# Optimization experiments

Measured on AMD Instinct MI355X. Metric: run time of the kernel, lower is better.

Reference implementation:

```python
import jax, jax.numpy as jnp
import numpy as np
from jax.scipy.special import logsumexp

VOCAB, EMB, SEQ = 100000, 300, 32768
NTAGS = 14          # 12 real tags + START + STOP
START, STOP = 12, 13
NEG = -10000.0


def setup_inputs() -> dict:
    key = jax.random.key(0)
    k0, k1, k2, k3, k4 = jax.random.split(key, 5)
    sentence = jax.random.randint(k0, (SEQ,), 0, VOCAB, dtype=jnp.int32)
    tags = jax.random.randint(k1, (SEQ,), 0, 12, dtype=jnp.int32)  # real tags only
    embeddings = jax.random.normal(k2, (VOCAB, EMB), dtype=jnp.float32)
    W = jax.random.normal(k3, (NTAGS, EMB), dtype=jnp.float32)  # linear2tag, no bias
    transitions = jax.random.normal(k4, (NTAGS, NTAGS), dtype=jnp.float32)
    # match __init__: no transition into START, none out of STOP
    transitions = transitions.at[START, :].set(NEG).at[:, STOP].set(NEG)
    return {"sentence": sentence, "tags": tags, "embeddings": embeddings,
            "W": W, "transitions": transitions}


def _forward_alg(feats, transitions):
    # feats: [L, T]; transitions[next, prev]
    init = jnp.full((NTAGS,), NEG, feats.dtype).at[START].set(0.0)

    def step(fv, feat):
        # alphas[next, prev] = fv[prev] + trans[next, prev] + feat[next]
        alphas = fv[None, :] + transitions + feat[:, None]
        return logsumexp(alphas, axis=1), None

    fv, _ = jax.lax.scan(step, init, feats)
    return logsumexp(fv + transitions[STOP])


def _score_sentence(feats, transitions, tags):
    prev = jnp.concatenate([jnp.array([START], tags.dtype), tags[:-1]])
    trans_score = jnp.sum(transitions[tags, prev])
    emit_score = jnp.sum(jnp.take_along_axis(feats, tags[:, None].astype(jnp.int32), axis=1))
    return trans_score + emit_score + transitions[STOP, tags[-1]]


def _viterbi(feats, transitions):
    init = jnp.full((NTAGS,), NEG, feats.dtype).at[START].set(0.0)

    def step(fv, feat):
        nv = fv[None, :] + transitions          # [next, prev]
        bp = jnp.argmax(nv, axis=1)             # best prev for each next
        return jnp.max(nv, axis=1) + feat, bp

    fv, bps = jax.lax.scan(step, init, feats)   # bps: [L, T]
    terminal = fv + transitions[STOP]
    best_last = jnp.argmax(terminal)
    path_score = terminal[best_last]

    def back(tag, bp):
        return bp[tag], tag                     # emit tag at this position

    _, path = jax.lax.scan(back, best_last, bps, reverse=True)  # [L]
    return path_score, path


def reference(sentence, tags, embeddings, W, transitions):
    # _get_features: embedding lookup + bias-free linear to tag space
    feats = embeddings[sentence] @ W.T                     # [L, T]
    forward_score = _forward_alg(feats, transitions)
    gold_score = _score_sentence(feats, transitions, tags)
    nll = forward_score - gold_score                       # neg_log_likelihood
    path_score, best_path = _viterbi(feats, transitions)   # module.forward
    return nll, path_score, best_path
```

## Files before the change

kernel.cpp:

```cpp
#include <hip/hip_runtime.h>


#define LSEQ    32768
#define NTAGS   14
#define R       12
#define T_START 12
#define T_STOP  13
#define EMBD    300
#define CCH     2048
#define SCH     16
#define NSUP    128
#define NHYP    8

#define OFF_FEATS 0
#define OFF_EXPF  393216
#define OFF_FMAX  786432
#define OFF_PF    819200
#define OFF_PV    1114112
#define OFF_PVC   1409024
#define OFF_BV    1703936
#define OFF_SFX   1728512
#define OFF_GOLD  1753088
#define OFF_SMV   1753104
#define OFF_SMVT  1771536
#define OFF_SMF   1789968
#define OFF_HMV   1808400
#define OFF_HMVT  1809552
#define OFF_HMF   1810704
#define OFF_SBV   1811856
#define OFF_SSFX  1813392
#define OFF_HBV   1814928
#define OFF_HSFX  1815024
#define OFF_GOLDP 1815120

__device__ __forceinline__ void load12(const float* __restrict__ p, float* r) {
  const float4* p4 = (const float4*)p;
  float4 a = p4[0], b = p4[1], c = p4[2];
  r[0]=a.x; r[1]=a.y; r[2]=a.z; r[3]=a.w;
  r[4]=b.x; r[5]=b.y; r[6]=b.z; r[7]=b.w;
  r[8]=c.x; r[9]=c.y; r[10]=c.z; r[11]=c.w;
}

__device__ __forceinline__ void lds12(const float* p, float* r) {
  const float4* p4 = (const float4*)p;
  float4 a = p4[0], b = p4[1], c = p4[2];
  r[0]=a.x; r[1]=a.y; r[2]=a.z; r[3]=a.w;
  r[4]=b.x; r[5]=b.y; r[6]=b.z; r[7]=b.w;
  r[8]=c.x; r[9]=c.y; r[10]=c.z; r[11]=c.w;
}

__global__ __launch_bounds__(256) void k_feats(
    const int* __restrict__ sentence, const int* __restrict__ tags,
    const float* __restrict__ emb, const float* __restrict__ W,
    const float* __restrict__ trans, float* __restrict__ ws)
{
  __shared__ float Wl[NTAGS * EMBD];
  __shared__ float gacc;
  for (int i = threadIdx.x; i < NTAGS * EMBD; i += 256) Wl[i] = W[i];
  if (threadIdx.x == 0) gacc = 0.f;
  __syncthreads();

  int grp = threadIdx.x >> 4;
  int g   = threadIdx.x & 15;
  int pos = blockIdx.x * 16 + grp;
  int row = sentence[pos];

  float acc = 0.f;
  if (g < R) {
    const float4* e4 = (const float4*)(emb + (size_t)row * EMBD);
    const float4* w4 = (const float4*)(Wl + g * EMBD);
    #pragma unroll 5
    for (int i = 0; i < EMBD / 4; ++i) {
      float4 a = e4[i]; float4 b = w4[i];
      acc += a.x*b.x + a.y*b.y + a.z*b.z + a.w*b.w;
    }
  }
  float feat = (g < R) ? acc : -3.0e38f;
  float mx = feat;
  #pragma unroll
  for (int off = 1; off < 16; off <<= 1)
    mx = fmaxf(mx, __shfl_xor(mx, off, 16));

  if (g < R) {
    ws[OFF_FEATS + pos * 12 + g] = feat;
    ws[OFF_EXPF  + pos * 12 + g] = __expf(feat - mx);
  }
  if (g == 0) ws[OFF_FMAX + pos] = mx;

  int tg = tags[pos];
  if (g == tg) {
    int prev = (pos == 0) ? T_START : tags[pos - 1];
    float gc = feat + trans[tg * NTAGS + prev];
    if (pos == LSEQ - 1) gc += trans[T_STOP * NTAGS + tg];
    atomicAdd(&gacc, gc);
  }
  __syncthreads();
  if (threadIdx.x == 0) ws[OFF_GOLDP + blockIdx.x] = gacc;
}

__global__ __launch_bounds__(64) void k_pass1(
    const float* __restrict__ trans, float* __restrict__ ws)
{
  int role = blockIdx.x >> 9;
  int q = threadIdx.x >> 4;
  int p = threadIdx.x & 15;
  int c = (blockIdx.x & 511) * 4 + q;
  int t0 = (c == 0) ? 1 : c * SCH;
  int t1 = c * SCH + SCH;
  bool act = (p < R);

  float Treg[R][R];

  if (role == 0) {
    #pragma unroll
    for (int n = 0; n < R; ++n)
      #pragma unroll
      for (int m = 0; m < R; ++m)
        Treg[n][m] = __expf(trans[n * NTAGS + m]);

    float E[R];
    #pragma unroll
    for (int m = 0; m < R; ++m) E[m] = (m == p) ? 1.f : 0.f;
    int kacc = 0;
    float sfeat = 0.f;

    float ef[R];
    load12(ws + OFF_EXPF + t0 * 12, ef);
    float fm = ws[OFF_FMAX + t0];

    for (int t = t0; t < t1; ++t) {
      float efn[R];
      load12(ws + OFF_EXPF + (t + 1) * 12, efn);
      float fmn = ws[OFF_FMAX + t + 1];
      sfeat += fm;
      float NE[R];
      #pragma unroll
      for (int n = 0; n < R; ++n) {
        float s = Treg[n][0] * E[0];
        #pragma unroll
        for (int m = 1; m < R; ++m) s = fmaf(Treg[n][m], E[m], s);
        NE[n] = s * ef[n];
      }
      #pragma unroll
      for (int n = 0; n < R; ++n) E[n] = NE[n];
      if ((t & 7) == 7) {
        float mx = E[0];
        #pragma unroll
        for (int n = 1; n < R; ++n) mx = fmaxf(mx, E[n]);
        if (mx > 0.f) {
          int k = ((__float_as_int(mx) >> 23) & 0xFF) - 127;
          float sc = __int_as_float((127 - k) << 23);
          #pragma unroll
          for (int n = 0; n < R; ++n) E[n] *= sc;
          kacc += k;
        }
      }
      #pragma unroll
      for (int n = 0; n < R; ++n) ef[n] = efn[n];
      fm = fmn;
    }
    if (act) {
      float base = (float)kacc * 0.6931471805599453f + sfeat;
      #pragma unroll
      for (int n = 0; n < R; ++n) {
        float v = (E[n] > 0.f) ? (__logf(E[n]) + base) : -1.0e30f;
        ws[OFF_PF + c * 144 + n * 12 + p] = v;
      }
    }
  } else {
    #pragma unroll
    for (int n = 0; n < R; ++n)
      #pragma unroll
      for (int m = 0; m < R; ++m)
        Treg[n][m] = trans[n * NTAGS + m];

    float V[R];
    #pragma unroll
    for (int m = 0; m < R; ++m) V[m] = (m == p) ? 0.f : -1.0e30f;

    float fr[R];
    load12(ws + OFF_FEATS + t0 * 12, fr);

    for (int t = t0; t < t1; ++t) {
      float frn[R];
      load12(ws + OFF_FEATS + (t + 1) * 12, frn);
      float NV[R];
      #pragma unroll
      for (int n = 0; n < R; ++n) {
        float b = Treg[n][0] + V[0];
        #pragma unroll
        for (int m = 1; m < R; ++m) b = fmaxf(b, Treg[n][m] + V[m]);
        NV[n] = b + fr[n];
      }
      #pragma unroll
      for (int n = 0; n < R; ++n) { V[n] = NV[n]; fr[n] = frn[n]; }
    }
    if (act) {
      #pragma unroll
      for (int n = 0; n < R; ++n) {
        ws[OFF_PV  + c * 144 + n * 12 + p] = V[n];
        ws[OFF_PVC + c * 144 + p * 12 + n] = V[n];
      }
    }
  }
}

__global__ __launch_bounds__(192) void k_foldS(
    float* __restrict__ ws, int srcV, int srcF, int dstV, int dstVT, int dstF)
{
  __shared__ float Msh[16 * 144];
  __shared__ float Vl[144];
  int s   = blockIdx.x >> 1;
  int sem = blockIdx.x & 1;
  int l = threadIdx.x;
  bool act = (l < 144);
  int n = l / 12;
  int p = l - n * 12;
  int base = sem ? srcF : srcV;

  const float4* src4 = (const float4*)(ws + base + s * (16 * 144));
  float4* d4 = (float4*)Msh;
  #pragma unroll
  for (int i = 0; i < 3; ++i) d4[l + i * 192] = src4[l + i * 192];

  float V = (act && n == p) ? 0.f : -1.0e30f;
  __syncthreads();

  for (int j = 0; j < 16; ++j) {
    if (act) Vl[l] = V;
    __syncthreads();
    if (act) {
      const float* M = Msh + j * 144 + n * 12;
      if (sem == 0) {
        float best = -3.0e38f;
        #pragma unroll
        for (int m = 0; m < R; ++m)
          best = fmaxf(best, M[m] + Vl[m * 12 + p]);
        V = best;
      } else {
        float cand[R]; float mx = -3.0e38f;
        #pragma unroll
        for (int m = 0; m < R; ++m) {
          cand[m] = M[m] + Vl[m * 12 + p];
          mx = fmaxf(mx, cand[m]);
        }
        float sum = 0.f;
        #pragma unroll
        for (int m = 0; m < R; ++m) sum += __expf(cand[m] - mx);
        V = mx + __logf(sum);
      }
    }
    __syncthreads();
  }
  if (act) {
    if (sem == 0) {
      ws[dstV  + s * 144 + n * 12 + p] = V;
      ws[dstVT + s * 144 + p * 12 + n] = V;
    } else {
      ws[dstF + s * 144 + n * 12 + p] = V;
    }
  }
}

__global__ __launch_bounds__(256) void k_midexpA(
    const float* __restrict__ trans, float* __restrict__ ws,
    float* __restrict__ out)
{
  __shared__ float hbv_sh[NHYP][12];
  __shared__ float hsfx_sh[NHYP][12];
  __shared__ float Vm[3][16];
  __shared__ float VexA[16][16];
  __shared__ float gold_sh, lse_sh;

  int tid  = threadIdx.x;
  int wid  = tid >> 6;
  int lane = tid & 63;

  if (wid == 0) {
    int n = lane; bool act = (n < R);
    float x = -3.0e38f;
    if (act) {
      x = trans[n * NTAGS + T_START] + ws[OFF_FEATS + n];
      hbv_sh[0][n] = x;
      Vm[0][n] = x;
    }
    float row[R], rown[R];
    if (act) load12(ws + OFF_HMV + n * 12, row);
    for (int h = 0; h < NHYP; ++h) {
      if (act) load12(ws + OFF_HMV + (h + 1) * 144 + n * 12, rown);
      float v[R];
      lds12(Vm[0], v);
      if (act) {
        float nx = row[0] + v[0];
        #pragma unroll
        for (int m = 1; m < R; ++m) nx = fmaxf(nx, row[m] + v[m]);
        if (h < NHYP - 1) hbv_sh[h + 1][n] = nx;
        Vm[0][n] = nx;
        #pragma unroll
        for (int m = 0; m < R; ++m) row[m] = rown[m];
      }
    }
    if (lane == 0) {
      float v[R];
      lds12(Vm[0], v);
      float ps = -3.0e38f;
      #pragma unroll
      for (int m = 0; m < R; ++m) ps = fmaxf(ps, v[m] + trans[T_STOP * NTAGS + m]);
      out[1] = ps;
    }
  } else if (wid == 1) {
    int n = lane; bool act = (n < R);
    float x = -3.0e38f;
    if (act) {
      x = trans[T_STOP * NTAGS + n];
      hsfx_sh[NHYP - 1][n] = x;
      Vm[1][n] = x;
    }
    float row[R], rown[R];
    if (act) load12(ws + OFF_HMVT + (NHYP - 1) * 144 + n * 12, row);
    for (int h = NHYP - 1; h >= 1; --h) {
      if (act) load12(ws + OFF_HMVT + (h - 1) * 144 + n * 12, rown);
      float v[R];
      lds12(Vm[1], v);
      if (act) {
        float nx = row[0] + v[0];
        #pragma unroll
        for (int m = 1; m < R; ++m) nx = fmaxf(nx, row[m] + v[m]);
        hsfx_sh[h - 1][n] = nx;
        Vm[1][n] = nx;
        #pragma unroll
        for (int m = 0; m < R; ++m) row[m] = rown[m];
      }
    }
  } else if (wid == 2) {
    int n = lane; bool act = (n < R);
    float x = -3.0e38f;
    if (act) {
      x = trans[n * NTAGS + T_START] + ws[OFF_FEATS + n];
      Vm[2][n] = x;
    }
    float row[R], rown[R];
    if (act) load12(ws + OFF_HMF + n * 12, row);
    for (int h = 0; h < NHYP; ++h) {
      if (act) load12(ws + OFF_HMF + (h + 1) * 144 + n * 12, rown);
      float v[R];
      lds12(Vm[2], v);
      if (act) {
        float tv[R]; float mx = -3.0e38f;
        #pragma unroll
        for (int m = 0; m < R; ++m) { tv[m] = row[m] + v[m]; mx = fmaxf(mx, tv[m]); }
        float sum = 0.f;
        #pragma unroll
        for (int m = 0; m < R; ++m) sum += __expf(tv[m] - mx);
        Vm[2][n] = mx + __logf(sum);
        #pragma unroll
        for (int m = 0; m < R; ++m) row[m] = rown[m];
      }
    }
    if (lane == 0) {
      float v[R];
      lds12(Vm[2], v);
      float mx = -3.0e38f;
      #pragma unroll
      for (int m = 0; m < R; ++m) mx = fmaxf(mx, v[m] + trans[T_STOP * NTAGS + m]);
      float sum = 0.f;
      #pragma unroll
      for (int m = 0; m < R; ++m) sum += __expf(v[m] + trans[T_STOP * NTAGS + m] - mx);
      lse_sh = mx + __logf(sum);
    }
  } else {
    float s = 0.f;
    for (int i = lane; i < CCH; i += 64) s += ws[OFF_GOLDP + i];
    #pragma unroll
    for (int off = 32; off > 0; off >>= 1) s += __shfl_xor(s, off);
    if (lane == 0) gold_sh = s;
  }
  __syncthreads();

  if (tid == 0) out[0] = lse_sh - gold_sh;

  {
    int dir  = tid >> 7;
    int h    = (tid >> 4) & 7;
    int g    = tid & 15;
    int task = tid >> 4;
    bool act = (g < R);

    if (dir == 0) {
      float x = -3.0e38f;
      if (act) {
        x = hbv_sh[h][g];
        ws[OFF_SBV + (h * 16) * 12 + g] = x;
        VexA[task][g] = x;
      }
      float row[R], rown[R];
      if (act) load12(ws + OFF_SMV + (h * 16) * 144 + g * 12, row);
      for (int j = 0; j < 15; ++j) {
        int s = h * 16 + j;
        if (act) load12(ws + OFF_SMV + (s + 1) * 144 + g * 12, rown);
        float v[R];
        lds12(VexA[task], v);
        if (act) {
          float nx = row[0] + v[0];
          #pragma unroll
          for (int m = 1; m < R; ++m) nx = fmaxf(nx, row[m] + v[m]);
          ws[OFF_SBV + (s + 1) * 12 + g] = nx;
          VexA[task][g] = nx;
          #pragma unroll
          for (int m = 0; m < R; ++m) row[m] = rown[m];
        }
      }
    } else {
      float x = -3.0e38f;
      if (act) {
        x = hsfx_sh[h][g];
        ws[OFF_SSFX + (h * 16 + 15) * 12 + g] = x;
        VexA[task][g] = x;
      }
      float row[R], rown[R];
      if (act) load12(ws + OFF_SMVT + (h * 16 + 15) * 144 + g * 12, row);
      for (int j = 15; j >= 1; --j) {
        int s = h * 16 + j;
        if (act) load12(ws + OFF_SMVT + (s - 1) * 144 + g * 12, rown);
        float v[R];
        lds12(VexA[task], v);
        if (act) {
          float nx = row[0] + v[0];
          #pragma unroll
          for (int m = 1; m < R; ++m) nx = fmaxf(nx, row[m] + v[m]);
          ws[OFF_SSFX + (s - 1) * 12 + g] = nx;
          VexA[task][g] = nx;
          #pragma unroll
          for (int m = 0; m < R; ++m) row[m] = rown[m];
        }
      }
    }
  }
}

__global__ __launch_bounds__(256) void k_expBdec(
    const float* __restrict__ trans, const float* __restrict__ ws,
    float* __restrict__ out)
{
  __shared__ float bv_sh[SCH][12];
  __shared__ float sfx_sh[SCH][12];
  __shared__ float Vdec[SCH][16];
  __shared__ unsigned char bpd[SCH][SCH][16];

  int tid = threadIdx.x;
  int s   = blockIdx.x;

  if (tid < 16) {
    int g = tid; bool act = (g < R);
    float x = -3.0e38f;
    if (act) { x = ws[OFF_SBV + s * 12 + g]; bv_sh[0][g] = x; }
    float row[R], rown[R];
    if (act) load12(ws + OFF_PV + (s * 16) * 144 + g * 12, row);
    for (int j = 0; j < 15; ++j) {
      if (act) load12(ws + OFF_PV + (s * 16 + j + 1) * 144 + g * 12, rown);
      float v[R];
      lds12(bv_sh[j], v);
      if (act) {
        float nx = row[0] + v[0];
        #pragma unroll
        for (int m = 1; m < R; ++m) nx = fmaxf(nx, row[m] + v[m]);
        bv_sh[j + 1][g] = nx;
        #pragma unroll
        for (int m = 0; m < R; ++m) row[m] = rown[m];
      }
    }
  } else if (tid >= 64 && tid < 80) {
    int g = tid - 64; bool act = (g < R);
    float x = -3.0e38f;
    if (act) { x = ws[OFF_SSFX + s * 12 + g]; sfx_sh[SCH - 1][g] = x; }
    float row[R], rown[R];
    if (act) load12(ws + OFF_PVC + (s * 16 + 15) * 144 + g * 12, row);
    for (int j = 15; j >= 1; --j) {
      if (act) load12(ws + OFF_PVC + (s * 16 + j - 1) * 144 + g * 12, rown);
      float v[R];
      lds12(sfx_sh[j], v);
      if (act) {
        float nx = row[0] + v[0];
        #pragma unroll
        for (int m = 1; m < R; ++m) nx = fmaxf(nx, row[m] + v[m]);
        sfx_sh[j - 1][g] = nx;
        #pragma unroll
        for (int m = 0; m < R; ++m) row[m] = rown[m];
      }
    }
  }
  __syncthreads();

  {
    int q = tid >> 4;
    int g = tid & 15;
    int c = s * 16 + q;
    int t0 = (c == 0) ? 1 : c * SCH;
    int t1 = c * SCH + SCH;
    bool act = (g < R);

    float treg[R];
    #pragma unroll
    for (int m = 0; m < R; ++m) treg[m] = act ? trans[g * NTAGS + m] : 0.f;

    float fv = act ? bv_sh[q][g] : -3.0e38f;
    Vdec[q][g] = fv;
    float fc = ws[OFF_FEATS + t0 * 12 + g];

    for (int t = t0; t < t1; ++t) {
      float fn = ws[OFF_FEATS + (t + 1) * 12 + g];
      float v[R];
      lds12(Vdec[q], v);
      float best = -3.0e38f; int bi = 0;
      #pragma unroll
      for (int m = 0; m < R; ++m) {
        float cand = treg[m] + v[m];
        if (cand > best) { best = cand; bi = m; }
      }
      float nfv = best + fc;
      if (act) {
        bpd[q][t - t0][g] = (unsigned char)bi;
        Vdec[q][g] = nfv;
      }
      fc = fn;
    }

    Vdec[q][g] = act ? (Vdec[q][g] + sfx_sh[q][g]) : -3.0e38f;

    if (g == 0) {
      float best = Vdec[q][0]; int idx = 0;
      #pragma unroll
      for (int m = 1; m < R; ++m) {
        float v = Vdec[q][m];
        if (v > best) { best = v; idx = m; }
      }
      int cur = idx;
      int len = t1 - t0;
      out[2 + t0 + len - 1] = (float)cur;
      for (int tt = len - 1; tt >= 1; --tt) {
        cur = bpd[q][tt][cur];
        out[2 + t0 + tt - 1] = (float)cur;
      }
      if (c == 0) {
        cur = bpd[q][0][cur];
        out[2 + 0] = (float)cur;
      }
    }
  }
}

extern "C" void kernel_launch(void* const* d_in, const int* in_sizes, int n_in,
                              void* d_out, int out_size, void* d_ws, size_t ws_size,
                              hipStream_t stream) {
  (void)in_sizes; (void)n_in; (void)out_size; (void)ws_size;
  const int*   sentence = (const int*)d_in[0];
  const int*   tags     = (const int*)d_in[1];
  const float* emb      = (const float*)d_in[2];
  const float* W        = (const float*)d_in[3];
  const float* trans    = (const float*)d_in[4];
  float* ws  = (float*)d_ws;
  float* out = (float*)d_out;

  k_feats<<<LSEQ / 16, 256, 0, stream>>>(sentence, tags, emb, W, trans, ws);
  k_pass1<<<1024, 64, 0, stream>>>(trans, ws);
  k_foldS<<<NSUP * 2, 192, 0, stream>>>(ws, OFF_PV, OFF_PF, OFF_SMV, OFF_SMVT, OFF_SMF);
  k_foldS<<<NHYP * 2, 192, 0, stream>>>(ws, OFF_SMV, OFF_SMF, OFF_HMV, OFF_HMVT, OFF_HMF);
  k_midexpA<<<1, 256, 0, stream>>>(trans, ws, out);
  k_expBdec<<<NSUP, 256, 0, stream>>>(trans, ws, out);
}
```

Before: 244.4 us.

## Fuse chunk scan with superchunk fold and replace hierarchical middle scan with flat scan

The per-chunk pass is fused with the first-level fold, so each 256-thread block computes 16 chunk matrices, stages them in shared memory and folds them in place. This removes the separate fold kernel and its global round trip. The second-level fold over 8 groups and the two-level middle scan are replaced by one sequential 128-step scan per direction that broadcasts state with wave shuffles instead of shared memory. This cuts two kernel launches and a level of hierarchy, but the middle scan becomes a longer serial chain run by a single wave each.

New measurement: 286.5 us. 17.2% more time.

```diff
diff --git a/kernel.cpp b/kernel.cpp
--- a/kernel.cpp
+++ b/kernel.cpp
@@ -10,7 +10,6 @@
 #define CCH     2048
 #define SCH     16
 #define NSUP    128
-#define NHYP    8
 
 #define OFF_FEATS 0
 #define OFF_EXPF  393216
@@ -25,12 +24,8 @@
 #define OFF_SMVT  1771536
 #define OFF_SMF   1789968
 #define OFF_HMV   1808400
-#define OFF_HMVT  1809552
-#define OFF_HMF   1810704
 #define OFF_SBV   1811856
 #define OFF_SSFX  1813392
-#define OFF_HBV   1814928
-#define OFF_HSFX  1815024
 #define OFF_GOLDP 1815120
 
 __device__ __forceinline__ void load12(const float* __restrict__ p, float* r) {
@@ -47,6 +42,13 @@
   r[0]=a.x; r[1]=a.y; r[2]=a.z; r[3]=a.w;
   r[4]=b.x; r[5]=b.y; r[6]=b.z; r[7]=b.w;
   r[8]=c.x; r[9]=c.y; r[10]=c.z; r[11]=c.w;
+}
+
+__device__ __forceinline__ float tmax12(const float* t) {
+  float a = fmaxf(fmaxf(t[0], t[1]), fmaxf(t[2], t[3]));
+  float b = fmaxf(fmaxf(t[4], t[5]), fmaxf(t[6], t[7]));
+  float c = fmaxf(fmaxf(t[8], t[9]), fmaxf(t[10], t[11]));
+  return fmaxf(fmaxf(a, b), c);
 }
 
 __global__ __launch_bounds__(256) void k_feats(
@@ -98,20 +100,25 @@
   if (threadIdx.x == 0) ws[OFF_GOLDP + blockIdx.x] = gacc;
 }
 
-__global__ __launch_bounds__(64) void k_pass1(
+__global__ __launch_bounds__(256, 1) void k_pass1f(
     const float* __restrict__ trans, float* __restrict__ ws)
 {
-  int role = blockIdx.x >> 9;
-  int q = threadIdx.x >> 4;
-  int p = threadIdx.x & 15;
-  int c = (blockIdx.x & 511) * 4 + q;
+  __shared__ float Msh[16 * 144];
+  __shared__ float Vl[144];
+
+  int tid = threadIdx.x;
+  int sem = blockIdx.x >> 7;
+  int s   = blockIdx.x & 127;
+  int q = tid >> 4;
+  int p = tid & 15;
+  int c = s * 16 + q;
   int t0 = (c == 0) ? 1 : c * SCH;
   int t1 = c * SCH + SCH;
   bool act = (p < R);
 
   float Treg[R][R];
 
-  if (role == 0) {
+  if (sem == 0) {
     #pragma unroll
     for (int n = 0; n < R; ++n)
       #pragma unroll
@@ -136,10 +143,10 @@
       float NE[R];
       #pragma unroll
       for (int n = 0; n < R; ++n) {
-        float s = Treg[n][0] * E[0];
-        #pragma unroll
-        for (int m = 1; m < R; ++m) s = fmaf(Treg[n][m], E[m], s);
-        NE[n] = s * ef[n];
+        float sv = Treg[n][0] * E[0];
+        #pragma unroll
+        for (int m = 1; m < R; ++m) sv = fmaf(Treg[n][m], E[m], sv);
+        NE[n] = sv * ef[n];
       }
       #pragma unroll
       for (int n = 0; n < R; ++n) E[n] = NE[n];
@@ -165,6 +172,7 @@
       for (int n = 0; n < R; ++n) {
         float v = (E[n] > 0.f) ? (__logf(E[n]) + base) : -1.0e30f;
         ws[OFF_PF + c * 144 + n * 12 + p] = v;
+        Msh[q * 144 + n * 12 + p] = v;
       }
     }
   } else {
@@ -200,242 +208,152 @@
       for (int n = 0; n < R; ++n) {
         ws[OFF_PV  + c * 144 + n * 12 + p] = V[n];
         ws[OFF_PVC + c * 144 + p * 12 + n] = V[n];
-      }
-    }
-  }
-}
-
-__global__ __launch_bounds__(192) void k_foldS(
-    float* __restrict__ ws, int srcV, int srcF, int dstV, int dstVT, int dstF)
-{
-  __shared__ float Msh[16 * 144];
-  __shared__ float Vl[144];
-  int s   = blockIdx.x >> 1;
-  int sem = blockIdx.x & 1;
-  int l = threadIdx.x;
-  bool act = (l < 144);
-  int n = l / 12;
-  int p = l - n * 12;
-  int base = sem ? srcF : srcV;
-
-  const float4* src4 = (const float4*)(ws + base + s * (16 * 144));
-  float4* d4 = (float4*)Msh;
-  #pragma unroll
-  for (int i = 0; i < 3; ++i) d4[l + i * 192] = src4[l + i * 192];
-
-  float V = (act && n == p) ? 0.f : -1.0e30f;
+        Msh[q * 144 + n * 12 + p] = V[n];
+      }
+    }
+  }
   __syncthreads();
 
-  for (int j = 0; j < 16; ++j) {
-    if (act) Vl[l] = V;
-    __syncthreads();
-    if (act) {
-      const float* M = Msh + j * 144 + n * 12;
-      if (sem == 0) {
-        float best = -3.0e38f;
-        #pragma unroll
-        for (int m = 0; m < R; ++m)
-          best = fmaxf(best, M[m] + Vl[m * 12 + p]);
-        V = best;
+  {
+    int l = tid;
+    bool fa = (l < 144);
+    int fn = l / 12;
+    int fp = l - fn * 12;
+    float V = (fa && fn == fp) ? 0.f : -1.0e30f;
+
+    for (int j = 0; j < 16; ++j) {
+      if (fa) Vl[l] = V;
+      __syncthreads();
+      if (fa) {
+        const float* M = Msh + j * 144 + fn * 12;
+        if (sem == 1) {
+          float best = -3.0e38f;
+          #pragma unroll
+          for (int m = 0; m < R; ++m)
+            best = fmaxf(best, M[m] + Vl[m * 12 + fp]);
+          V = best;
+        } else {
+          float cand[R]; float mx = -3.0e38f;
+          #pragma unroll
+          for (int m = 0; m < R; ++m) {
+            cand[m] = M[m] + Vl[m * 12 + fp];
+            mx = fmaxf(mx, cand[m]);
+          }
+          float sum = 0.f;
+          #pragma unroll
+          for (int m = 0; m < R; ++m) sum += __expf(cand[m] - mx);
+          V = mx + __logf(sum);
+        }
+      }
+      __syncthreads();
+    }
+    if (fa) {
+      if (sem == 1) {
+        ws[OFF_SMV  + s * 144 + fn * 12 + fp] = V;
+        ws[OFF_SMVT + s * 144 + fp * 12 + fn] = V;
       } else {
-        float cand[R]; float mx = -3.0e38f;
-        #pragma unroll
-        for (int m = 0; m < R; ++m) {
-          cand[m] = M[m] + Vl[m * 12 + p];
-          mx = fmaxf(mx, cand[m]);
-        }
-        float sum = 0.f;
-        #pragma unroll
-        for (int m = 0; m < R; ++m) sum += __expf(cand[m] - mx);
-        V = mx + __logf(sum);
-      }
-    }
-    __syncthreads();
-  }
-  if (act) {
-    if (sem == 0) {
-      ws[dstV  + s * 144 + n * 12 + p] = V;
-      ws[dstVT + s * 144 + p * 12 + n] = V;
-    } else {
-      ws[dstF + s * 144 + n * 12 + p] = V;
-    }
-  }
-}
-
-__global__ __launch_bounds__(256) void k_midexpA(
+        ws[OFF_SMF + s * 144 + fn * 12 + fp] = V;
+      }
+    }
+  }
+}
+
+__global__ __launch_bounds__(256) void k_midS(
     const float* __restrict__ trans, float* __restrict__ ws,
     float* __restrict__ out)
 {
-  __shared__ float hbv_sh[NHYP][12];
-  __shared__ float hsfx_sh[NHYP][12];
-  __shared__ float Vm[3][16];
-  __shared__ float VexA[16][16];
   __shared__ float gold_sh, lse_sh;
-
   int tid  = threadIdx.x;
   int wid  = tid >> 6;
   int lane = tid & 63;
+  int n = lane;
+  bool act = (n < R);
 
   if (wid == 0) {
-    int n = lane; bool act = (n < R);
-    float x = -3.0e38f;
-    if (act) {
-      x = trans[n * NTAGS + T_START] + ws[OFF_FEATS + n];
-      hbv_sh[0][n] = x;
-      Vm[0][n] = x;
-    }
+    float v = act ? (trans[n * NTAGS + T_START] + ws[OFF_FEATS + n]) : -3.0e38f;
     float row[R], rown[R];
-    if (act) load12(ws + OFF_HMV + n * 12, row);
-    for (int h = 0; h < NHYP; ++h) {
-      if (act) load12(ws + OFF_HMV + (h + 1) * 144 + n * 12, rown);
-      float v[R];
-      lds12(Vm[0], v);
-      if (act) {
-        float nx = row[0] + v[0];
-        #pragma unroll
-        for (int m = 1; m < R; ++m) nx = fmaxf(nx, row[m] + v[m]);
-        if (h < NHYP - 1) hbv_sh[h + 1][n] = nx;
-        Vm[0][n] = nx;
+    if (act) load12(ws + OFF_SMV + n * 12, row);
+    for (int s = 0; s < NSUP; ++s) {
+      if (act) load12(ws + OFF_SMV + (s + 1) * 144 + n * 12, rown);
+      if (act) ws[OFF_SBV + s * 12 + n] = v;
+      float vb[R];
+      #pragma unroll
+      for (int m = 0; m < R; ++m) vb[m] = __shfl(v, m, 16);
+      if (act) {
+        float t[R];
+        #pragma unroll
+        for (int m = 0; m < R; ++m) t[m] = row[m] + vb[m];
+        v = tmax12(t);
         #pragma unroll
         for (int m = 0; m < R; ++m) row[m] = rown[m];
       }
     }
-    if (lane == 0) {
-      float v[R];
-      lds12(Vm[0], v);
-      float ps = -3.0e38f;
-      #pragma unroll
-      for (int m = 0; m < R; ++m) ps = fmaxf(ps, v[m] + trans[T_STOP * NTAGS + m]);
-      out[1] = ps;
-    }
+    float t = act ? (v + trans[T_STOP * NTAGS + n]) : -3.0e38f;
+    #pragma unroll
+    for (int off = 1; off < 16; off <<= 1)
+      t = fmaxf(t, __shfl_xor(t, off, 16));
+    if (lane == 0) out[1] = t;
   } else if (wid == 1) {
-    int n = lane; bool act = (n < R);
-    float x = -3.0e38f;
-    if (act) {
-      x = trans[T_STOP * NTAGS + n];
-      hsfx_sh[NHYP - 1][n] = x;
-      Vm[1][n] = x;
-    }
+    float u = act ? trans[T_STOP * NTAGS + n] : -3.0e38f;
+    if (act) ws[OFF_SSFX + (NSUP - 1) * 12 + n] = u;
     float row[R], rown[R];
-    if (act) load12(ws + OFF_HMVT + (NHYP - 1) * 144 + n * 12, row);
-    for (int h = NHYP - 1; h >= 1; --h) {
-      if (act) load12(ws + OFF_HMVT + (h - 1) * 144 + n * 12, rown);
-      float v[R];
-      lds12(Vm[1], v);
-      if (act) {
-        float nx = row[0] + v[0];
-        #pragma unroll
-        for (int m = 1; m < R; ++m) nx = fmaxf(nx, row[m] + v[m]);
-        hsfx_sh[h - 1][n] = nx;
-        Vm[1][n] = nx;
+    if (act) load12(ws + OFF_SMVT + (NSUP - 1) * 144 + n * 12, row);
+    for (int s = NSUP - 1; s >= 1; --s) {
+      if (act) load12(ws + OFF_SMVT + (s - 1) * 144 + n * 12, rown);
+      float ub[R];
+      #pragma unroll
+      for (int m = 0; m < R; ++m) ub[m] = __shfl(u, m, 16);
+      if (act) {
+        float t[R];
+        #pragma unroll
+        for (int m = 0; m < R; ++m) t[m] = row[m] + ub[m];
+        u = tmax12(t);
+        ws[OFF_SSFX + (s - 1) * 12 + n] = u;
         #pragma unroll
         for (int m = 0; m < R; ++m) row[m] = rown[m];
       }
     }
   } else if (wid == 2) {
-    int n = lane; bool act = (n < R);
-    float x = -3.0e38f;
-    if (act) {
-      x = trans[n * NTAGS + T_START] + ws[OFF_FEATS + n];
-      Vm[2][n] = x;
-    }
+    float w = act ? (trans[n * NTAGS + T_START] + ws[OFF_FEATS + n]) : -3.0e38f;
     float row[R], rown[R];
-    if (act) load12(ws + OFF_HMF + n * 12, row);
-    for (int h = 0; h < NHYP; ++h) {
-      if (act) load12(ws + OFF_HMF + (h + 1) * 144 + n * 12, rown);
-      float v[R];
-      lds12(Vm[2], v);
-      if (act) {
-        float tv[R]; float mx = -3.0e38f;
-        #pragma unroll
-        for (int m = 0; m < R; ++m) { tv[m] = row[m] + v[m]; mx = fmaxf(mx, tv[m]); }
+    if (act) load12(ws + OFF_SMF + n * 12, row);
+    for (int s = 0; s < NSUP; ++s) {
+      if (act) load12(ws + OFF_SMF + (s + 1) * 144 + n * 12, rown);
+      float wb[R];
+      #pragma unroll
+      for (int m = 0; m < R; ++m) wb[m] = __shfl(w, m, 16);
+      if (act) {
+        float t[R];
+        #pragma unroll
+        for (int m = 0; m < R; ++m) t[m] = row[m] + wb[m];
+        float mx = tmax12(t);
         float sum = 0.f;
         #pragma unroll
-        for (int m = 0; m < R; ++m) sum += __expf(tv[m] - mx);
-        Vm[2][n] = mx + __logf(sum);
+        for (int m = 0; m < R; ++m) sum += __expf(t[m] - mx);
+        w = mx + __logf(sum);
         #pragma unroll
         for (int m = 0; m < R; ++m) row[m] = rown[m];
       }
     }
-    if (lane == 0) {
-      float v[R];
-      lds12(Vm[2], v);
-      float mx = -3.0e38f;
-      #pragma unroll
-      for (int m = 0; m < R; ++m) mx = fmaxf(mx, v[m] + trans[T_STOP * NTAGS + m]);
-      float sum = 0.f;
-      #pragma unroll
-      for (int m = 0; m < R; ++m) sum += __expf(v[m] + trans[T_STOP * NTAGS + m] - mx);
-      lse_sh = mx + __logf(sum);
-    }
+    float t = act ? (w + trans[T_STOP * NTAGS + n]) : -3.0e38f;
+    float mx = t;
+    #pragma unroll
+    for (int off = 1; off < 16; off <<= 1)
+      mx = fmaxf(mx, __shfl_xor(mx, off, 16));
+    float e = act ? __expf(t - mx) : 0.f;
+    #pragma unroll
+    for (int off = 1; off < 16; off <<= 1)
+      e += __shfl_xor(e, off, 16);
+    if (lane == 0) lse_sh = mx + __logf(e);
   } else {
-    float s = 0.f;
-    for (int i = lane; i < CCH; i += 64) s += ws[OFF_GOLDP + i];
-    #pragma unroll
-    for (int off = 32; off > 0; off >>= 1) s += __shfl_xor(s, off);
-    if (lane == 0) gold_sh = s;
+    float sg = 0.f;
+    for (int i = lane; i < CCH; i += 64) sg += ws[OFF_GOLDP + i];
+    #pragma unroll
+    for (int off = 1; off < 64; off <<= 1) sg += __shfl_xor(sg, off);
+    if (lane == 0) gold_sh = sg;
   }
   __syncthreads();
-
   if (tid == 0) out[0] = lse_sh - gold_sh;
-
-  {
-    int dir  = tid >> 7;
-    int h    = (tid >> 4) & 7;
-    int g    = tid & 15;
-    int task = tid >> 4;
-    bool act = (g < R);
-
-    if (dir == 0) {
-      float x = -3.0e38f;
-      if (act) {
-        x = hbv_sh[h][g];
-        ws[OFF_SBV + (h * 16) * 12 + g] = x;
-        VexA[task][g] = x;
-      }
-      float row[R], rown[R];
-      if (act) load12(ws + OFF_SMV + (h * 16) * 144 + g * 12, row);
-      for (int j = 0; j < 15; ++j) {
-        int s = h * 16 + j;
-        if (act) load12(ws + OFF_SMV + (s + 1) * 144 + g * 12, rown);
-        float v[R];
-        lds12(VexA[task], v);
-        if (act) {
-          float nx = row[0] + v[0];
-          #pragma unroll
-          for (int m = 1; m < R; ++m) nx = fmaxf(nx, row[m] + v[m]);
-          ws[OFF_SBV + (s + 1) * 12 + g] = nx;
-          VexA[task][g] = nx;
-          #pragma unroll
-          for (int m = 0; m < R; ++m) row[m] = rown[m];
-        }
-      }
-    } else {
-      float x = -3.0e38f;
-      if (act) {
-        x = hsfx_sh[h][g];
-        ws[OFF_SSFX + (h * 16 + 15) * 12 + g] = x;
-        VexA[task][g] = x;
-      }
-      float row[R], rown[R];
-      if (act) load12(ws + OFF_SMVT + (h * 16 + 15) * 144 + g * 12, row);
-      for (int j = 15; j >= 1; --j) {
-        int s = h * 16 + j;
-        if (act) load12(ws + OFF_SMVT + (s - 1) * 144 + g * 12, rown);
-        float v[R];
-        lds12(VexA[task], v);
-        if (act) {
-          float nx = row[0] + v[0];
-          #pragma unroll
-          for (int m = 1; m < R; ++m) nx = fmaxf(nx, row[m] + v[m]);
-          ws[OFF_SSFX + (s - 1) * 12 + g] = nx;
-          VexA[task][g] = nx;
-          #pragma unroll
-          for (int m = 0; m < R; ++m) row[m] = rown[m];
-        }
-      }
-    }
-  }
 }
 
 __global__ __launch_bounds__(256) void k_expBdec(
@@ -562,9 +480,7 @@
   float* out = (float*)d_out;
 
   k_feats<<<LSEQ / 16, 256, 0, stream>>>(sentence, tags, emb, W, trans, ws);
-  k_pass1<<<1024, 64, 0, stream>>>(trans, ws);
-  k_foldS<<<NSUP * 2, 192, 0, stream>>>(ws, OFF_PV, OFF_PF, OFF_SMV, OFF_SMVT, OFF_SMF);
-  k_foldS<<<NHYP * 2, 192, 0, stream>>>(ws, OFF_SMV, OFF_SMF, OFF_HMV, OFF_HMVT, OFF_HMF);
-  k_midexpA<<<1, 256, 0, stream>>>(trans, ws, out);
+  k_pass1f<<<NSUP * 2, 256, 0, stream>>>(trans, ws);
+  k_midS<<<1, 256, 0, stream>>>(trans, ws, out);
   k_expBdec<<<NSUP, 256, 0, stream>>>(trans, ws, out);
 }
```

## Fuse chunk pass with superchunk fold and move hyperchunk fold into mid kernel

Applied to the files above, without the earlier changes.

The per-chunk scan kernel now uses 256-thread blocks covering 16 chunks each and folds the resulting 16 chunk matrices into a superchunk matrix in shared memory, removing the PF round trip and one fold launch. The single-block mid kernel loads all superchunk matrices into LDS, computes the 8 hyperchunk folds itself with per-thread register scans, and reads transposed views from LDS instead of separate transposed global copies. This cuts three launches down to two and removes global traffic, at the cost of a large LDS footprint and a longer serial single-block phase with lower per-block parallelism in pass1.

Result: slower. 277.3 us (+13.5%).

```diff
diff --git a/kernel.cpp b/kernel.cpp
--- a/kernel.cpp
+++ b/kernel.cpp
@@ -18,19 +18,11 @@
 #define OFF_PF    819200
 #define OFF_PV    1114112
 #define OFF_PVC   1409024
-#define OFF_BV    1703936
-#define OFF_SFX   1728512
-#define OFF_GOLD  1753088
 #define OFF_SMV   1753104
 #define OFF_SMVT  1771536
 #define OFF_SMF   1789968
-#define OFF_HMV   1808400
-#define OFF_HMVT  1809552
-#define OFF_HMF   1810704
 #define OFF_SBV   1811856
 #define OFF_SSFX  1813392
-#define OFF_HBV   1814928
-#define OFF_HSFX  1815024
 #define OFF_GOLDP 1815120
 
 __device__ __forceinline__ void load12(const float* __restrict__ p, float* r) {
@@ -98,20 +90,25 @@
   if (threadIdx.x == 0) ws[OFF_GOLDP + blockIdx.x] = gacc;
 }
 
-__global__ __launch_bounds__(64) void k_pass1(
+__global__ __launch_bounds__(256, 1) void k_pass1f(
     const float* __restrict__ trans, float* __restrict__ ws)
 {
-  int role = blockIdx.x >> 9;
-  int q = threadIdx.x >> 4;
-  int p = threadIdx.x & 15;
-  int c = (blockIdx.x & 511) * 4 + q;
+  __shared__ float Msh[16 * 144];
+  __shared__ float Vl[144];
+
+  int tid = threadIdx.x;
+  int sem = blockIdx.x >> 7;
+  int s   = blockIdx.x & 127;
+  int q = tid >> 4;
+  int p = tid & 15;
+  int c = s * 16 + q;
   int t0 = (c == 0) ? 1 : c * SCH;
   int t1 = c * SCH + SCH;
   bool act = (p < R);
 
   float Treg[R][R];
 
-  if (role == 0) {
+  if (sem == 0) {
     #pragma unroll
     for (int n = 0; n < R; ++n)
       #pragma unroll
@@ -136,10 +133,10 @@
       float NE[R];
       #pragma unroll
       for (int n = 0; n < R; ++n) {
-        float s = Treg[n][0] * E[0];
-        #pragma unroll
-        for (int m = 1; m < R; ++m) s = fmaf(Treg[n][m], E[m], s);
-        NE[n] = s * ef[n];
+        float sv = Treg[n][0] * E[0];
+        #pragma unroll
+        for (int m = 1; m < R; ++m) sv = fmaf(Treg[n][m], E[m], sv);
+        NE[n] = sv * ef[n];
       }
       #pragma unroll
       for (int n = 0; n < R; ++n) E[n] = NE[n];
@@ -164,7 +161,7 @@
       #pragma unroll
       for (int n = 0; n < R; ++n) {
         float v = (E[n] > 0.f) ? (__logf(E[n]) + base) : -1.0e30f;
-        ws[OFF_PF + c * 144 + n * 12 + p] = v;
+        Msh[q * 144 + n * 12 + p] = v;
       }
     }
   } else {
@@ -200,190 +197,227 @@
       for (int n = 0; n < R; ++n) {
         ws[OFF_PV  + c * 144 + n * 12 + p] = V[n];
         ws[OFF_PVC + c * 144 + p * 12 + n] = V[n];
-      }
-    }
-  }
-}
-
-__global__ __launch_bounds__(192) void k_foldS(
-    float* __restrict__ ws, int srcV, int srcF, int dstV, int dstVT, int dstF)
-{
-  __shared__ float Msh[16 * 144];
-  __shared__ float Vl[144];
-  int s   = blockIdx.x >> 1;
-  int sem = blockIdx.x & 1;
-  int l = threadIdx.x;
-  bool act = (l < 144);
-  int n = l / 12;
-  int p = l - n * 12;
-  int base = sem ? srcF : srcV;
-
-  const float4* src4 = (const float4*)(ws + base + s * (16 * 144));
-  float4* d4 = (float4*)Msh;
-  #pragma unroll
-  for (int i = 0; i < 3; ++i) d4[l + i * 192] = src4[l + i * 192];
-
-  float V = (act && n == p) ? 0.f : -1.0e30f;
-  __syncthreads();
-
-  for (int j = 0; j < 16; ++j) {
-    if (act) Vl[l] = V;
-    __syncthreads();
-    if (act) {
-      const float* M = Msh + j * 144 + n * 12;
-      if (sem == 0) {
-        float best = -3.0e38f;
-        #pragma unroll
-        for (int m = 0; m < R; ++m)
-          best = fmaxf(best, M[m] + Vl[m * 12 + p]);
-        V = best;
-      } else {
-        float cand[R]; float mx = -3.0e38f;
-        #pragma unroll
-        for (int m = 0; m < R; ++m) {
-          cand[m] = M[m] + Vl[m * 12 + p];
-          mx = fmaxf(mx, cand[m]);
-        }
-        float sum = 0.f;
-        #pragma unroll
-        for (int m = 0; m < R; ++m) sum += __expf(cand[m] - mx);
-        V = mx + __logf(sum);
-      }
-    }
-    __syncthreads();
-  }
-  if (act) {
-    if (sem == 0) {
-      ws[dstV  + s * 144 + n * 12 + p] = V;
-      ws[dstVT + s * 144 + p * 12 + n] = V;
-    } else {
-      ws[dstF + s * 144 + n * 12 + p] = V;
-    }
-  }
-}
-
-__global__ __launch_bounds__(256) void k_midexpA(
+        Msh[q * 144 + n * 12 + p] = V[n];
+      }
+    }
+  }
+  __syncthreads();
+
+  {
+    int l = tid;
+    bool fa = (l < 144);
+    int fn = l / 12;
+    int fp = l - fn * 12;
+    float V = (fa && fn == fp) ? 0.f : -1.0e30f;
+
+    for (int j = 0; j < 16; ++j) {
+      if (fa) Vl[l] = V;
+      __syncthreads();
+      if (fa) {
+        const float* M = Msh + j * 144 + fn * 12;
+        if (sem == 1) {
+          float best = -3.0e38f;
+          #pragma unroll
+          for (int m = 0; m < R; ++m)
+            best = fmaxf(best, M[m] + Vl[m * 12 + fp]);
+          V = best;
+        } else {
+          float cand[R]; float mx = -3.0e38f;
+          #pragma unroll
+          for (int m = 0; m < R; ++m) {
+            cand[m] = M[m] + Vl[m * 12 + fp];
+            mx = fmaxf(mx, cand[m]);
+          }
+          float sum = 0.f;
+          #pragma unroll
+          for (int m = 0; m < R; ++m) sum += __expf(cand[m] - mx);
+          V = mx + __logf(sum);
+        }
+      }
+      __syncthreads();
+    }
+    if (fa) {
+      if (sem == 1) ws[OFF_SMV + s * 144 + fn * 12 + fp] = V;
+      else          ws[OFF_SMF + s * 144 + fn * 12 + fp] = V;
+    }
+  }
+}
+
+__global__ __launch_bounds__(256) void k_midT(
     const float* __restrict__ trans, float* __restrict__ ws,
     float* __restrict__ out)
 {
+  __shared__ float Lsh[NSUP * 144 * 2 + NHYP * 144 * 2];
   __shared__ float hbv_sh[NHYP][12];
   __shared__ float hsfx_sh[NHYP][12];
   __shared__ float Vm[3][16];
   __shared__ float VexA[16][16];
+  __shared__ float gpart[64];
   __shared__ float gold_sh, lse_sh;
+
+  float* lsmv = Lsh;
+  float* lsmf = Lsh + NSUP * 144;
+  float* hmv  = Lsh + NSUP * 144 * 2;
+  float* hmf  = hmv + NHYP * 144;
 
   int tid  = threadIdx.x;
   int wid  = tid >> 6;
   int lane = tid & 63;
 
-  if (wid == 0) {
-    int n = lane; bool act = (n < R);
-    float x = -3.0e38f;
-    if (act) {
-      x = trans[n * NTAGS + T_START] + ws[OFF_FEATS + n];
-      hbv_sh[0][n] = x;
-      Vm[0][n] = x;
-    }
-    float row[R], rown[R];
-    if (act) load12(ws + OFF_HMV + n * 12, row);
-    for (int h = 0; h < NHYP; ++h) {
-      if (act) load12(ws + OFF_HMV + (h + 1) * 144 + n * 12, rown);
-      float v[R];
-      lds12(Vm[0], v);
-      if (act) {
-        float nx = row[0] + v[0];
-        #pragma unroll
-        for (int m = 1; m < R; ++m) nx = fmaxf(nx, row[m] + v[m]);
-        if (h < NHYP - 1) hbv_sh[h + 1][n] = nx;
-        Vm[0][n] = nx;
-        #pragma unroll
-        for (int m = 0; m < R; ++m) row[m] = rown[m];
-      }
-    }
-    if (lane == 0) {
-      float v[R];
-      lds12(Vm[0], v);
-      float ps = -3.0e38f;
-      #pragma unroll
-      for (int m = 0; m < R; ++m) ps = fmaxf(ps, v[m] + trans[T_STOP * NTAGS + m]);
-      out[1] = ps;
-    }
-  } else if (wid == 1) {
-    int n = lane; bool act = (n < R);
-    float x = -3.0e38f;
-    if (act) {
-      x = trans[T_STOP * NTAGS + n];
-      hsfx_sh[NHYP - 1][n] = x;
-      Vm[1][n] = x;
-    }
-    float row[R], rown[R];
-    if (act) load12(ws + OFF_HMVT + (NHYP - 1) * 144 + n * 12, row);
-    for (int h = NHYP - 1; h >= 1; --h) {
-      if (act) load12(ws + OFF_HMVT + (h - 1) * 144 + n * 12, rown);
-      float v[R];
-      lds12(Vm[1], v);
-      if (act) {
-        float nx = row[0] + v[0];
-        #pragma unroll
-        for (int m = 1; m < R; ++m) nx = fmaxf(nx, row[m] + v[m]);
-        hsfx_sh[h - 1][n] = nx;
-        Vm[1][n] = nx;
-        #pragma unroll
-        for (int m = 0; m < R; ++m) row[m] = rown[m];
-      }
-    }
-  } else if (wid == 2) {
-    int n = lane; bool act = (n < R);
-    float x = -3.0e38f;
-    if (act) {
-      x = trans[n * NTAGS + T_START] + ws[OFF_FEATS + n];
-      Vm[2][n] = x;
-    }
-    float row[R], rown[R];
-    if (act) load12(ws + OFF_HMF + n * 12, row);
-    for (int h = 0; h < NHYP; ++h) {
-      if (act) load12(ws + OFF_HMF + (h + 1) * 144 + n * 12, rown);
-      float v[R];
-      lds12(Vm[2], v);
-      if (act) {
-        float tv[R]; float mx = -3.0e38f;
-        #pragma unroll
-        for (int m = 0; m < R; ++m) { tv[m] = row[m] + v[m]; mx = fmaxf(mx, tv[m]); }
-        float sum = 0.f;
-        #pragma unroll
-        for (int m = 0; m < R; ++m) sum += __expf(tv[m] - mx);
-        Vm[2][n] = mx + __logf(sum);
-        #pragma unroll
-        for (int m = 0; m < R; ++m) row[m] = rown[m];
-      }
-    }
-    if (lane == 0) {
-      float v[R];
-      lds12(Vm[2], v);
-      float mx = -3.0e38f;
-      #pragma unroll
-      for (int m = 0; m < R; ++m) mx = fmaxf(mx, v[m] + trans[T_STOP * NTAGS + m]);
-      float sum = 0.f;
-      #pragma unroll
-      for (int m = 0; m < R; ++m) sum += __expf(v[m] + trans[T_STOP * NTAGS + m] - mx);
-      lse_sh = mx + __logf(sum);
-    }
-  } else {
-    float s = 0.f;
-    for (int i = lane; i < CCH; i += 64) s += ws[OFF_GOLDP + i];
+  {
+    const float4* a4 = (const float4*)(ws + OFF_SMV);
+    const float4* b4 = (const float4*)(ws + OFF_SMF);
+    float4* d0 = (float4*)lsmv;
+    float4* d1 = (float4*)lsmf;
+    for (int i = tid; i < NSUP * 36; i += 256) { d0[i] = a4[i]; d1[i] = b4[i]; }
+    if (wid == 3) {
+      float sg = 0.f;
+      for (int i = lane; i < CCH; i += 64) sg += ws[OFF_GOLDP + i];
+      gpart[lane] = sg;
+    }
+  }
+  __syncthreads();
+
+  {
+    int t    = tid >> 4;
+    int p    = tid & 15;
+    int kind = t >> 3;
+    int h    = t & 7;
+    float A[R];
     #pragma unroll
-    for (int off = 32; off > 0; off >>= 1) s += __shfl_xor(s, off);
-    if (lane == 0) gold_sh = s;
-  }
-  __syncthreads();
-
+    for (int m = 0; m < R; ++m) A[m] = (m == p) ? 0.f : -1.0e30f;
+    const float* base = kind ? lsmf : lsmv;
+    for (int j = 0; j < 16; ++j) {
+      const float* M = base + (h * 16 + j) * 144;
+      float NA[R];
+      if (kind == 0) {
+        #pragma unroll
+        for (int n = 0; n < R; ++n) {
+          float b = M[n * 12] + A[0];
+          #pragma unroll
+          for (int m = 1; m < R; ++m) b = fmaxf(b, M[n * 12 + m] + A[m]);
+          NA[n] = b;
+        }
+      } else {
+        #pragma unroll
+        for (int n = 0; n < R; ++n) {
+          float cand[R]; float mx = -3.0e38f;
+          #pragma unroll
+          for (int m = 0; m < R; ++m) {
+            cand[m] = M[n * 12 + m] + A[m];
+            mx = fmaxf(mx, cand[m]);
+          }
+          float sum = 0.f;
+          #pragma unroll
+          for (int m = 0; m < R; ++m) sum += __expf(cand[m] - mx);
+          NA[n] = mx + __logf(sum);
+        }
+      }
+      #pragma unroll
+      for (int n = 0; n < R; ++n) A[n] = NA[n];
+    }
+    if (p < R) {
+      float* dst = kind ? (hmf + h * 144) : (hmv + h * 144);
+      #pragma unroll
+      for (int n = 0; n < R; ++n) dst[n * 12 + p] = A[n];
+    }
+  }
+  __syncthreads();
+
+  {
+    int n = lane;
+    bool act = (n < R);
+    if (wid == 0) {
+      float x = -3.0e38f;
+      if (act) {
+        x = trans[n * NTAGS + T_START] + ws[OFF_FEATS + n];
+        hbv_sh[0][n] = x;
+        Vm[0][n] = x;
+      }
+      for (int h = 0; h < NHYP; ++h) {
+        float row[R], v[R];
+        if (act) lds12(hmv + h * 144 + n * 12, row);
+        lds12(Vm[0], v);
+        if (act) {
+          float nx = row[0] + v[0];
+          #pragma unroll
+          for (int m = 1; m < R; ++m) nx = fmaxf(nx, row[m] + v[m]);
+          if (h < NHYP - 1) hbv_sh[h + 1][n] = nx;
+          Vm[0][n] = nx;
+        }
+      }
+      float t2 = act ? (Vm[0][n] + trans[T_STOP * NTAGS + n]) : -3.0e38f;
+      #pragma unroll
+      for (int off = 1; off < 16; off <<= 1)
+        t2 = fmaxf(t2, __shfl_xor(t2, off, 16));
+      if (lane == 0) out[1] = t2;
+    } else if (wid == 1) {
+      float x = -3.0e38f;
+      if (act) {
+        x = trans[T_STOP * NTAGS + n];
+        hsfx_sh[NHYP - 1][n] = x;
+        Vm[1][n] = x;
+      }
+      for (int h = NHYP - 1; h >= 1; --h) {
+        float row[R], v[R];
+        if (act) {
+          #pragma unroll
+          for (int m = 0; m < R; ++m) row[m] = hmv[h * 144 + m * 12 + n];
+        }
+        lds12(Vm[1], v);
+        if (act) {
+          float nx = row[0] + v[0];
+          #pragma unroll
+          for (int m = 1; m < R; ++m) nx = fmaxf(nx, row[m] + v[m]);
+          hsfx_sh[h - 1][n] = nx;
+          Vm[1][n] = nx;
+        }
+      }
+    } else if (wid == 2) {
+      float x = -3.0e38f;
+      if (act) {
+        x = trans[n * NTAGS + T_START] + ws[OFF_FEATS + n];
+        Vm[2][n] = x;
+      }
+      for (int h = 0; h < NHYP; ++h) {
+        float row[R], v[R];
+        if (act) lds12(hmf + h * 144 + n * 12, row);
+        lds12(Vm[2], v);
+        if (act) {
+          float tv[R]; float mx = -3.0e38f;
+          #pragma unroll
+          for (int m = 0; m < R; ++m) { tv[m] = row[m] + v[m]; mx = fmaxf(mx, tv[m]); }
+          float sum = 0.f;
+          #pragma unroll
+          for (int m = 0; m < R; ++m) sum += __expf(tv[m] - mx);
+          Vm[2][n] = mx + __logf(sum);
+        }
+      }
+      float t2 = act ? (Vm[2][n] + trans[T_STOP * NTAGS + n]) : -3.0e38f;
+      float mx = t2;
+      #pragma unroll
+      for (int off = 1; off < 16; off <<= 1)
+        mx = fmaxf(mx, __shfl_xor(mx, off, 16));
+      float e = act ? __expf(t2 - mx) : 0.f;
+      #pragma unroll
+      for (int off = 1; off < 16; off <<= 1)
+        e += __shfl_xor(e, off, 16);
+      if (lane == 0) lse_sh = mx + __logf(e);
+    } else {
+      float sg = gpart[lane];
+      #pragma unroll
+      for (int off = 1; off < 64; off <<= 1) sg += __shfl_xor(sg, off);
+      if (lane == 0) gold_sh = sg;
+    }
+  }
+  __syncthreads();
   if (tid == 0) out[0] = lse_sh - gold_sh;
 
   {
     int dir  = tid >> 7;
-    int h    = (tid >> 4) & 7;
+    int task = tid >> 4;
+    int h    = task & 7;
     int g    = tid & 15;
-    int task = tid >> 4;
     bool act = (g < R);
 
     if (dir == 0) {
@@ -393,12 +427,10 @@
         ws[OFF_SBV + (h * 16) * 12 + g] = x;
         VexA[task][g] = x;
       }
-      float row[R], rown[R];
-      if (act) load12(ws + OFF_SMV + (h * 16) * 144 + g * 12, row);
       for (int j = 0; j < 15; ++j) {
         int s = h * 16 + j;
-        if (act) load12(ws + OFF_SMV + (s + 1) * 144 + g * 12, rown);
-        float v[R];
+        float row[R], v[R];
+        if (act) lds12(lsmv + s * 144 + g * 12, row);
         lds12(VexA[task], v);
         if (act) {
           float nx = row[0] + v[0];
@@ -406,8 +438,6 @@
           for (int m = 1; m < R; ++m) nx = fmaxf(nx, row[m] + v[m]);
           ws[OFF_SBV + (s + 1) * 12 + g] = nx;
           VexA[task][g] = nx;
-          #pragma unroll
-          for (int m = 0; m < R; ++m) row[m] = rown[m];
         }
       }
     } else {
@@ -417,12 +447,13 @@
         ws[OFF_SSFX + (h * 16 + 15) * 12 + g] = x;
         VexA[task][g] = x;
       }
-      float row[R], rown[R];
-      if (act) load12(ws + OFF_SMVT + (h * 16 + 15) * 144 + g * 12, row);
       for (int j = 15; j >= 1; --j) {
         int s = h * 16 + j;
-        if (act) load12(ws + OFF_SMVT + (s - 1) * 144 + g * 12, rown);
-        float v[R];
+        float row[R], v[R];
+        if (act) {
+          #pragma unroll
+          for (int m = 0; m < R; ++m) row[m] = lsmv[s * 144 + m * 12 + g];
+        }
         lds12(VexA[task], v);
         if (act) {
           float nx = row[0] + v[0];
@@ -430,8 +461,6 @@
           for (int m = 1; m < R; ++m) nx = fmaxf(nx, row[m] + v[m]);
           ws[OFF_SSFX + (s - 1) * 12 + g] = nx;
           VexA[task][g] = nx;
-          #pragma unroll
-          for (int m = 0; m < R; ++m) row[m] = rown[m];
         }
       }
     }
@@ -562,9 +591,7 @@
   float* out = (float*)d_out;
 
   k_feats<<<LSEQ / 16, 256, 0, stream>>>(sentence, tags, emb, W, trans, ws);
-  k_pass1<<<1024, 64, 0, stream>>>(trans, ws);
-  k_foldS<<<NSUP * 2, 192, 0, stream>>>(ws, OFF_PV, OFF_PF, OFF_SMV, OFF_SMVT, OFF_SMF);
-  k_foldS<<<NHYP * 2, 192, 0, stream>>>(ws, OFF_SMV, OFF_SMF, OFF_HMV, OFF_HMVT, OFF_HMF);
-  k_midexpA<<<1, 256, 0, stream>>>(trans, ws, out);
+  k_pass1f<<<NSUP * 2, 256, 0, stream>>>(trans, ws);
+  k_midT<<<1, 256, 0, stream>>>(trans, ws, out);
   k_expBdec<<<NSUP, 256, 0, stream>>>(trans, ws, out);
 }
```

## Fuse chunk pass1 with first-level fold into one kernel

Applied to the files above, without the earlier changes.

Merges the per-chunk transfer-matrix pass and the first super-chunk fold into a single kernel. Each block now handles 16 chunks of one semiring and folds their 12x12 matrices in shared memory, skipping the global write and re-read of the forward matrices and one kernel launch. In exchange the grid drops from 1024 blocks of 64 threads to 256 blocks of 256 threads, which lowers parallelism. It also adds a serial 16-step fold with barriers inside each block.

Result: no change. 240.1 us (-1.8%).

```diff
diff --git a/kernel.cpp b/kernel.cpp
--- a/kernel.cpp
+++ b/kernel.cpp
@@ -18,9 +18,6 @@
 #define OFF_PF    819200
 #define OFF_PV    1114112
 #define OFF_PVC   1409024
-#define OFF_BV    1703936
-#define OFF_SFX   1728512
-#define OFF_GOLD  1753088
 #define OFF_SMV   1753104
 #define OFF_SMVT  1771536
 #define OFF_SMF   1789968
@@ -29,8 +26,6 @@
 #define OFF_HMF   1810704
 #define OFF_SBV   1811856
 #define OFF_SSFX  1813392
-#define OFF_HBV   1814928
-#define OFF_HSFX  1815024
 #define OFF_GOLDP 1815120
 
 __device__ __forceinline__ void load12(const float* __restrict__ p, float* r) {
@@ -98,20 +93,25 @@
   if (threadIdx.x == 0) ws[OFF_GOLDP + blockIdx.x] = gacc;
 }
 
-__global__ __launch_bounds__(64) void k_pass1(
+__global__ __launch_bounds__(256, 1) void k_pass1f(
     const float* __restrict__ trans, float* __restrict__ ws)
 {
-  int role = blockIdx.x >> 9;
-  int q = threadIdx.x >> 4;
-  int p = threadIdx.x & 15;
-  int c = (blockIdx.x & 511) * 4 + q;
+  __shared__ float Msh[16 * 144];
+  __shared__ float Vl[144];
+
+  int tid = threadIdx.x;
+  int sem = blockIdx.x >> 7;
+  int s   = blockIdx.x & 127;
+  int q = tid >> 4;
+  int p = tid & 15;
+  int c = s * 16 + q;
   int t0 = (c == 0) ? 1 : c * SCH;
   int t1 = c * SCH + SCH;
   bool act = (p < R);
 
   float Treg[R][R];
 
-  if (role == 0) {
+  if (sem == 0) {
     #pragma unroll
     for (int n = 0; n < R; ++n)
       #pragma unroll
@@ -136,10 +136,10 @@
       float NE[R];
       #pragma unroll
       for (int n = 0; n < R; ++n) {
-        float s = Treg[n][0] * E[0];
-        #pragma unroll
-        for (int m = 1; m < R; ++m) s = fmaf(Treg[n][m], E[m], s);
-        NE[n] = s * ef[n];
+        float sv = Treg[n][0] * E[0];
+        #pragma unroll
+        for (int m = 1; m < R; ++m) sv = fmaf(Treg[n][m], E[m], sv);
+        NE[n] = sv * ef[n];
       }
       #pragma unroll
       for (int n = 0; n < R; ++n) E[n] = NE[n];
@@ -164,7 +164,7 @@
       #pragma unroll
       for (int n = 0; n < R; ++n) {
         float v = (E[n] > 0.f) ? (__logf(E[n]) + base) : -1.0e30f;
-        ws[OFF_PF + c * 144 + n * 12 + p] = v;
+        Msh[q * 144 + n * 12 + p] = v;
       }
     }
   } else {
@@ -200,6 +200,51 @@
       for (int n = 0; n < R; ++n) {
         ws[OFF_PV  + c * 144 + n * 12 + p] = V[n];
         ws[OFF_PVC + c * 144 + p * 12 + n] = V[n];
+        Msh[q * 144 + n * 12 + p] = V[n];
+      }
+    }
+  }
+  __syncthreads();
+
+  {
+    int l = tid;
+    bool fa = (l < 144);
+    int fn = l / 12;
+    int fp = l - fn * 12;
+    float V = (fa && fn == fp) ? 0.f : -1.0e30f;
+
+    for (int j = 0; j < 16; ++j) {
+      if (fa) Vl[l] = V;
+      __syncthreads();
+      if (fa) {
+        const float* M = Msh + j * 144 + fn * 12;
+        if (sem == 1) {
+          float best = -3.0e38f;
+          #pragma unroll
+          for (int m = 0; m < R; ++m)
+            best = fmaxf(best, M[m] + Vl[m * 12 + fp]);
+          V = best;
+        } else {
+          float cand[R]; float mx = -3.0e38f;
+          #pragma unroll
+          for (int m = 0; m < R; ++m) {
+            cand[m] = M[m] + Vl[m * 12 + fp];
+            mx = fmaxf(mx, cand[m]);
+          }
+          float sum = 0.f;
+          #pragma unroll
+          for (int m = 0; m < R; ++m) sum += __expf(cand[m] - mx);
+          V = mx + __logf(sum);
+        }
+      }
+      __syncthreads();
+    }
+    if (fa) {
+      if (sem == 1) {
+        ws[OFF_SMV  + s * 144 + fn * 12 + fp] = V;
+        ws[OFF_SMVT + s * 144 + fp * 12 + fn] = V;
+      } else {
+        ws[OFF_SMF + s * 144 + fn * 12 + fp] = V;
       }
     }
   }
@@ -562,8 +607,7 @@
   float* out = (float*)d_out;
 
   k_feats<<<LSEQ / 16, 256, 0, stream>>>(sentence, tags, emb, W, trans, ws);
-  k_pass1<<<1024, 64, 0, stream>>>(trans, ws);
-  k_foldS<<<NSUP * 2, 192, 0, stream>>>(ws, OFF_PV, OFF_PF, OFF_SMV, OFF_SMVT, OFF_SMF);
+  k_pass1f<<<NSUP * 2, 256, 0, stream>>>(trans, ws);
   k_foldS<<<NHYP * 2, 192, 0, stream>>>(ws, OFF_SMV, OFF_SMF, OFF_HMV, OFF_HMVT, OFF_HMF);
   k_midexpA<<<1, 256, 0, stream>>>(trans, ws, out);
   k_expBdec<<<NSUP, 256, 0, stream>>>(trans, ws, out);
```
